# Optimization experiments

Measured on AMD Instinct MI355X. Metric: run time of the kernel, lower is better.

Reference implementation:

```python
import jax, jax.numpy as jnp
import numpy as np

DIM = 128
NUM_ROT = DIM * (DIM - 1) // 2  # 8128
# Strict upper-triangular pairs in row-major order: i outer, j from i+1 (matches the torch loop)
_PI, _PJ = np.triu_indices(DIM, k=1)


def setup_inputs() -> dict:
    key = jax.random.key(0)
    k1, k2 = jax.random.split(key)
    x = jax.random.normal(k1, (32, 4096, DIM), dtype=jnp.float32)
    angles = jax.random.normal(k2, (NUM_ROT,), dtype=jnp.float32) * 0.01
    bias = jnp.zeros((DIM,), dtype=jnp.float32)
    return {"x": x, "angles": angles, "bias": bias}


def reference(x, angles, bias):
    # Sequential Givens plane rotations applied in pair order (read-after-write chain),
    # expressed as a lax.scan carrying the full vector batch.
    cos_vals = jnp.cos(angles)
    sin_vals = jnp.sin(angles)
    ii = jnp.asarray(_PI, dtype=jnp.int32)
    jj = jnp.asarray(_PJ, dtype=jnp.int32)

    def step(out, cs):
        c, s, i, j = cs
        xi = out[..., i]  # [B, S]
        xj = out[..., j]
        out = out.at[..., i].set(c * xi - s * xj).at[..., j].set(s * xi + c * xj)
        return out, None

    out, _ = jax.lax.scan(step, x, (cos_vals, sin_vals, ii, jj))
    return out + bias
```

## Files before the change

kernel.cpp:

```cpp
#include <hip/hip_runtime.h>
#include <hip/hip_bf16.h>

#define DIM 128

typedef __attribute__((ext_vector_type(4))) float f32x4;
typedef __attribute__((ext_vector_type(8))) short bf16x8;

__device__ __forceinline__ unsigned short f2bf(float f) {
  union { float f; unsigned int u; } v; v.f = f;
  unsigned int u = v.u;
  return (unsigned short)((u + 0x7FFFu + ((u >> 16) & 1u)) >> 16);
}

template<int LO, int NF, int N, int RB, int RE>
__device__ void build_group(const float* __restrict__ angles, float* __restrict__ A,
                            float4* __restrict__ cs) {
  const int t = threadIdx.x;
  for (int r0 = RB + t; r0 < RE; r0 += 256) {
    int i = (int)floorf((255.0f - sqrtf(65025.0f - 8.0f * (float)r0)) * 0.5f);
    if (i < 0) i = 0; if (i > 126) i = 126;
    while (127 * (i + 1) - ((i + 1) * i) / 2 <= r0) ++i;
    while (127 * i - (i * (i - 1)) / 2 > r0) --i;
    const int Ti = 127 * i - (i * (i - 1)) / 2;
    const int j  = i + 1 + (r0 - Ti);
    const int fl = i - LO, p = fl >> 1, sec = fl & 1;
    const int f1 = 2 * p;
    const int off = p * (N - p) + ((j - LO) - f1 - 1);
    float s, c; __sincosf(angles[r0], &s, &c);
    float2 v; v.x = c; v.y = s;
    *((float2*)&cs[off] + sec) = v;
  }
  __syncthreads();
  if (t >= N) return;

  float col[N];
  #pragma unroll
  for (int r = 0; r < N; ++r) col[r] = (r == t) ? 1.0f : 0.0f;

  constexpr int P = (NF + 1) / 2;
  #pragma unroll
  for (int p = 0; p < P; ++p) {
    const int f1 = 2 * p;
    const float4 e0 = cs[p * (N - p)];
    float r1 = col[f1];
    const float rj = col[f1 + 1];
    float r2 = fmaf(e0.y, r1, e0.x * rj);
    r1 = fmaf(e0.x, r1, -(e0.y * rj));
    #pragma unroll
    for (int jl = f1 + 2; jl < N; ++jl) {
      const float4 e = cs[p * (N - p) + (jl - f1 - 1)];
      const float rv = col[jl];
      const float wv = fmaf(e.y, r1, e.x * rv);
      r1 = fmaf(e.x, r1, -(e.y * rv));
      col[jl] = fmaf(e.w, r2, e.z * wv);
      r2 = fmaf(e.z, r2, -(e.w * wv));
    }
    col[f1] = r1; col[f1 + 1] = r2;
  }
  #pragma unroll
  for (int r = 0; r < N; ++r) A[r * N + t] = col[r];
}

__global__ __launch_bounds__(256, 1) void k_build(const float* __restrict__ angles,
                                                  float* __restrict__ ws) {
  __shared__ float4 cs[1104];
  const int t = threadIdx.x;
  for (int k = t; k < 1104; k += 256) { float4 v; v.x = 1.f; v.y = 0.f; v.z = 1.f; v.w = 0.f; cs[k] = v; }
  __syncthreads();
  switch (blockIdx.x) {
    case 0: build_group<0, 17, 128,    0, 2023>(angles, ws,         cs); break;
    case 1: build_group<17, 21, 111, 2023, 4123>(angles, ws + 16384, cs); break;
    case 2: build_group<38, 26,  90, 4123, 6112>(angles, ws + 28705, cs); break;
    default: build_group<64, 63, 64, 6112, 8128>(angles, ws + 36805, cs); break;
  }
}

__global__ __launch_bounds__(128) void k_combine(const float* __restrict__ ws,
                                                 unsigned short* __restrict__ Mb) {
  __shared__ float x[DIM];
  const int c = blockIdx.x, r = threadIdx.x;
  x[r] = (r == c) ? 1.0f : 0.0f;
  __syncthreads();
  const int LOs[4]  = {0, 17, 38, 64};
  const int Ns[4]   = {128, 111, 90, 64};
  const int offs[4] = {0, 16384, 28705, 36805};
  #pragma unroll
  for (int g = 0; g < 4; ++g) {
    const int lo = LOs[g], n = Ns[g];
    float y;
    if (r >= lo) {
      const float* Ar = ws + offs[g] + (r - lo) * n;
      float acc = 0.0f;
      #pragma unroll 8
      for (int k = 0; k < n; ++k) acc = fmaf(Ar[k], x[lo + k], acc);
      y = acc;
    } else {
      y = x[r];
    }
    __syncthreads();
    x[r] = y;
    __syncthreads();
  }
  Mb[r * DIM + c] = f2bf(x[r]);
}

__global__ __launch_bounds__(256) void k_gemm(const float* __restrict__ X,
                                              const float* __restrict__ bias,
                                              const unsigned short* __restrict__ Mb,
                                              float* __restrict__ out) {
  const int lane = threadIdx.x & 63;
  const int wid  = threadIdx.x >> 6;
  const int l15  = lane & 15, lhi = lane >> 4;
  const int rowbase = blockIdx.x * 128 + wid * 32;

  f32x4 acc[2][8];
  #pragma unroll
  for (int m = 0; m < 2; ++m)
    #pragma unroll
    for (int n = 0; n < 8; ++n) acc[m][n] = (f32x4){0.f, 0.f, 0.f, 0.f};

  bf16x8 a[2][4];
  #pragma unroll
  for (int mt = 0; mt < 2; ++mt) {
    const float* xp = X + (rowbase + mt * 16 + l15) * DIM + lhi * 8;
    #pragma unroll
    for (int kt = 0; kt < 4; ++kt) {
      const f32x4 x0 = *(const f32x4*)(xp + kt * 32);
      const f32x4 x1 = *(const f32x4*)(xp + kt * 32 + 4);
      bf16x8 av;
      av[0] = (short)f2bf(x0[0]); av[1] = (short)f2bf(x0[1]);
      av[2] = (short)f2bf(x0[2]); av[3] = (short)f2bf(x0[3]);
      av[4] = (short)f2bf(x1[0]); av[5] = (short)f2bf(x1[1]);
      av[6] = (short)f2bf(x1[2]); av[7] = (short)f2bf(x1[3]);
      a[mt][kt] = av;
    }
  }

  #pragma unroll
  for (int kt = 0; kt < 4; ++kt) {
    #pragma unroll
    for (int n = 0; n < 8; ++n) {
      const bf16x8 b = *(const bf16x8*)(Mb + ((l15 + 16 * n) * DIM + kt * 32 + lhi * 8));
      acc[0][n] = __builtin_amdgcn_mfma_f32_16x16x32_bf16(a[0][kt], b, acc[0][n], 0, 0, 0);
      acc[1][n] = __builtin_amdgcn_mfma_f32_16x16x32_bf16(a[1][kt], b, acc[1][n], 0, 0, 0);
    }
  }

  #pragma unroll
  for (int n = 0; n < 8; ++n) {
    const float bs = bias[16 * n + l15];
    #pragma unroll
    for (int mt = 0; mt < 2; ++mt) {
      const int rb = rowbase + mt * 16 + lhi * 4;
      #pragma unroll
      for (int j = 0; j < 4; ++j)
        out[(rb + j) * DIM + 16 * n + l15] = acc[mt][n][j] + bs;
    }
  }
}

extern "C" void kernel_launch(void* const* d_in, const int* in_sizes, int n_in,
                              void* d_out, int out_size, void* d_ws, size_t ws_size,
                              hipStream_t stream) {
  const float* x      = (const float*)d_in[0];
  const float* angles = (const float*)d_in[1];
  const float* bias   = (const float*)d_in[2];
  float* out = (float*)d_out;
  float* ws  = (float*)d_ws;
  unsigned short* Mb = (unsigned short*)((char*)d_ws + 163616);

  k_build<<<4, 256, 0, stream>>>(angles, ws);
  k_combine<<<128, 128, 0, stream>>>(ws, Mb);
  k_gemm<<<1024, 256, 0, stream>>>(x, bias, Mb, out);
}
```

Baseline: 91.54 us.

## Stage X tile via LDS async loads and move build columns to shared memory

The GEMM kernel now copies each 128x128 fp32 X tile into LDS using global_load_lds with an XOR-swizzled layout, then reads the A fragments from LDS instead of making strided 16-byte global loads. The rotation-build kernel keeps each thread's column in shared memory instead of a fully unrolled register array, processing rotations in 16-wide chunks with a new padded coefficient layout. This aims to get coalesced global reads in the GEMM and to cut register pressure and code size in the build. The cost is 64KB of LDS per GEMM block, which limits occupancy, and an extra barrier before compute starts.

```diff
diff --git a/kernel.cpp b/kernel.cpp
--- a/kernel.cpp
+++ b/kernel.cpp
@@ -12,10 +12,24 @@
   return (unsigned short)((u + 0x7FFFu + ((u >> 16) & 1u)) >> 16);
 }
 
-template<int LO, int NF, int N, int RB, int RE>
+__device__ __forceinline__ void load_lds16(const float* src, float* dst) {
+  __builtin_amdgcn_global_load_lds((const __attribute__((address_space(1))) void*)src,
+                                   (__attribute__((address_space(3))) void*)dst, 16, 0, 0);
+}
+
+__device__ __forceinline__ int pair_start(int p) { return 2 * p + ((p & 1) << 1); }
+__device__ __forceinline__ int pair_Lp(int N, int p) {
+  const int fp = (p & 1) ? 0 : 2;
+  const int len = N - 2 * p - 2;
+  return (fp + len + 15) & ~15;
+}
+
+template<int LO, int N, int P, int RB, int RE>
 __device__ void build_group(const float* __restrict__ angles, float* __restrict__ A,
-                            float4* __restrict__ cs) {
+                            float* __restrict__ col, float4* __restrict__ cs) {
   const int t = threadIdx.x;
+  for (int k = t; k < 1248; k += 256) { float4 v; v.x = 1.f; v.y = 0.f; v.z = 1.f; v.w = 0.f; cs[k] = v; }
+  __syncthreads();
   for (int r0 = RB + t; r0 < RE; r0 += 256) {
     int i = (int)floorf((255.0f - sqrtf(65025.0f - 8.0f * (float)r0)) * 0.5f);
     if (i < 0) i = 0; if (i > 126) i = 126;
@@ -24,54 +38,68 @@
     const int Ti = 127 * i - (i * (i - 1)) / 2;
     const int j  = i + 1 + (r0 - Ti);
     const int fl = i - LO, p = fl >> 1, sec = fl & 1;
-    const int f1 = 2 * p;
-    const int off = p * (N - p) + ((j - LO) - f1 - 1);
+    int bp = 0;
+    for (int q = 0; q < p; ++q) bp += 1 + pair_Lp(N, q);
     float s, c; __sincosf(angles[r0], &s, &c);
-    float2 v; v.x = c; v.y = s;
-    *((float2*)&cs[off] + sec) = v;
+    const int jloc = j - LO;
+    if (sec == 0 && jloc == 2 * p + 1) {
+      *(float2*)&cs[bp] = (float2){c, s};
+    } else {
+      const int slot = bp + 1 + (jloc - pair_start(p));
+      *((float2*)&cs[slot] + sec) = (float2){c, s};
+    }
   }
   __syncthreads();
   if (t >= N) return;
 
-  float col[N];
-  #pragma unroll
-  for (int r = 0; r < N; ++r) col[r] = (r == t) ? 1.0f : 0.0f;
-
-  constexpr int P = (NF + 1) / 2;
-  #pragma unroll
+  float* myc = col + t * 148;
+  for (int r = 0; r < 148; ++r) myc[r] = (r == t) ? 1.0f : 0.0f;
+
+  int base = 0;
+  #pragma unroll 1
   for (int p = 0; p < P; ++p) {
     const int f1 = 2 * p;
-    const float4 e0 = cs[p * (N - p)];
-    float r1 = col[f1];
-    const float rj = col[f1 + 1];
+    const int st = pair_start(p);
+    const int Lp = pair_Lp(N, p);
+    const float4 e0 = cs[base];
+    float r1 = myc[f1];
+    const float rj = myc[f1 + 1];
     float r2 = fmaf(e0.y, r1, e0.x * rj);
     r1 = fmaf(e0.x, r1, -(e0.y * rj));
-    #pragma unroll
-    for (int jl = f1 + 2; jl < N; ++jl) {
-      const float4 e = cs[p * (N - p) + (jl - f1 - 1)];
-      const float rv = col[jl];
-      const float wv = fmaf(e.y, r1, e.x * rv);
-      r1 = fmaf(e.x, r1, -(e.y * rv));
-      col[jl] = fmaf(e.w, r2, e.z * wv);
-      r2 = fmaf(e.z, r2, -(e.w * wv));
-    }
-    col[f1] = r1; col[f1 + 1] = r2;
-  }
-  #pragma unroll
-  for (int r = 0; r < N; ++r) A[r * N + t] = col[r];
+    #pragma unroll 1
+    for (int jb = 0; jb < Lp; jb += 16) {
+      f32x4 v[4]; float4 e[16];
+      #pragma unroll
+      for (int q = 0; q < 4; ++q) v[q] = *(f32x4*)&myc[st + jb + 4 * q];
+      #pragma unroll
+      for (int q = 0; q < 16; ++q) e[q] = cs[base + 1 + jb + q];
+      #pragma unroll
+      for (int q = 0; q < 16; ++q) {
+        const float rv = v[q >> 2][q & 3];
+        const float wv = fmaf(e[q].y, r1, e[q].x * rv);
+        r1 = fmaf(e[q].x, r1, -(e[q].y * rv));
+        v[q >> 2][q & 3] = fmaf(e[q].w, r2, e[q].z * wv);
+        r2 = fmaf(e[q].z, r2, -(e[q].w * wv));
+      }
+      #pragma unroll
+      for (int q = 0; q < 4; ++q) *(f32x4*)&myc[st + jb + 4 * q] = v[q];
+    }
+    myc[f1] = r1;
+    myc[f1 + 1] = r2;
+    base += 1 + Lp;
+  }
+  for (int r = 0; r < N; ++r) A[r * N + t] = myc[r];
 }
 
 __global__ __launch_bounds__(256, 1) void k_build(const float* __restrict__ angles,
                                                   float* __restrict__ ws) {
-  __shared__ float4 cs[1104];
-  const int t = threadIdx.x;
-  for (int k = t; k < 1104; k += 256) { float4 v; v.x = 1.f; v.y = 0.f; v.z = 1.f; v.w = 0.f; cs[k] = v; }
-  __syncthreads();
+  __shared__ float  col[128 * 148];
+  __shared__ float4 cs[1248];
   switch (blockIdx.x) {
-    case 0: build_group<0, 17, 128,    0, 2023>(angles, ws,         cs); break;
-    case 1: build_group<17, 21, 111, 2023, 4123>(angles, ws + 16384, cs); break;
-    case 2: build_group<38, 26,  90, 4123, 6112>(angles, ws + 28705, cs); break;
-    default: build_group<64, 63, 64, 6112, 8128>(angles, ws + 36805, cs); break;
+    case 0: build_group< 0, 128,  9,    0, 2023>(angles, ws,         col, cs); break;
+    case 1: build_group<17, 111, 11, 2023, 4123>(angles, ws + 16384, col, cs); break;
+    case 2: build_group<38,  90, 13, 4123, 6112>(angles, ws + 28705, col, cs); break;
+    default: build_group<64, 64, 32, 6112, 8128>(angles, ws + 36805, col, cs); break;
   }
 }
 
@@ -108,10 +136,20 @@
                                               const float* __restrict__ bias,
                                               const unsigned short* __restrict__ Mb,
                                               float* __restrict__ out) {
-  const int lane = threadIdx.x & 63;
-  const int wid  = threadIdx.x >> 6;
-  const int l15  = lane & 15, lhi = lane >> 4;
-  const int rowbase = blockIdx.x * 128 + wid * 32;
+  __shared__ float Xs[128 * 128];
+  const int t = threadIdx.x;
+  const int lane = t & 63, wid = t >> 6;
+  const int l15 = lane & 15, lhi = lane >> 4;
+  const float* Xblk = X + (size_t)blockIdx.x * 16384;
+
+  #pragma unroll
+  for (int it = 0; it < 16; ++it) {
+    const int g = (it * 4 + wid) * 64 + lane;
+    const int r = g >> 5, kc = g & 31;
+    const int pu = (kc >> 1) ^ (r & 15), h = kc & 1;
+    load_lds16(Xblk + r * 128 + pu * 8 + h * 4, &Xs[(it * 4 + wid) * 256]);
+  }
+  __syncthreads();
 
   f32x4 acc[2][8];
   #pragma unroll
@@ -122,11 +160,13 @@
   bf16x8 a[2][4];
   #pragma unroll
   for (int mt = 0; mt < 2; ++mt) {
-    const float* xp = X + (rowbase + mt * 16 + l15) * DIM + lhi * 8;
+    const int r = wid * 32 + mt * 16 + l15;
     #pragma unroll
     for (int kt = 0; kt < 4; ++kt) {
-      const f32x4 x0 = *(const f32x4*)(xp + kt * 32);
-      const f32x4 x1 = *(const f32x4*)(xp + kt * 32 + 4);
+      const int pu = (kt * 4 + lhi) ^ (r & 15);
+      const float* p = &Xs[r * 128 + pu * 8];
+      const f32x4 x0 = *(const f32x4*)p;
+      const f32x4 x1 = *(const f32x4*)(p + 4);
       bf16x8 av;
       av[0] = (short)f2bf(x0[0]); av[1] = (short)f2bf(x0[1]);
       av[2] = (short)f2bf(x0[2]); av[3] = (short)f2bf(x0[3]);
@@ -146,6 +186,7 @@
     }
   }
 
+  const int rowbase = blockIdx.x * 128 + wid * 32;
   #pragma unroll
   for (int n = 0; n < 8; ++n) {
     const float bs = bias[16 * n + l15];
```

Result: slower. 108.7 us (+18.7%).

## Split rotation matrix build into 32 groups and shrink GEMM tiles

Applied to the files above, without the earlier changes.

The Givens rotation chain is now split into 32 groups built in parallel blocks, up from 4, with each block's partial rotation matrix accumulated in shared memory. The output buffer serves as scratch for these partial matrices. k_combine now multiplies through 32 padded partial matrices using vectorized loads. The GEMM uses one 16-row tile per wave with more blocks and a higher occupancy hint. The aim is to cut the serial latency of the small-grid build kernel, in exchange for more combine steps and shared-memory traffic.

```diff
diff --git a/kernel.cpp b/kernel.cpp
--- a/kernel.cpp
+++ b/kernel.cpp
@@ -2,9 +2,20 @@
 #include <hip/hip_bf16.h>
 
 #define DIM 128
+#define G 32
 
 typedef __attribute__((ext_vector_type(4))) float f32x4;
 typedef __attribute__((ext_vector_type(8))) short bf16x8;
+
+__device__ const int LOt[G + 1] = {
+  0,2,4,6,8,10,13,15,17,19,22,24,27,29,32,35,37,40,43,46,49,53,56,60,64,68,72,77,82,88,95,105,127};
+__device__ const int RBt[G + 1] = {
+  0,253,502,747,988,1225,1573,1800,2023,2242,2563,2772,3078,3277,3568,3850,4033,4300,4558,4807,
+  5047,5353,5572,5850,6112,6358,6588,6853,7093,7348,7600,7875,8128};
+__device__ const int AOFFt[G + 1] = {
+  0,16384,32512,47888,63016,77416,91576,104916,118024,130456,142664,154112,164928,175432,185332,
+  194548,203476,211848,219592,227072,233960,240280,245980,251164,255788,259884,263484,266620,
+  269272,271480,273080,274268,274820};
 
 __device__ __forceinline__ unsigned short f2bf(float f) {
   union { float f; unsigned int u; } v; v.f = f;
@@ -12,90 +23,100 @@
   return (unsigned short)((u + 0x7FFFu + ((u >> 16) & 1u)) >> 16);
 }
 
-template<int LO, int NF, int N, int RB, int RE>
-__device__ void build_group(const float* __restrict__ angles, float* __restrict__ A,
-                            float4* __restrict__ cs) {
+__global__ __launch_bounds__(256) void k_build(const float* __restrict__ angles,
+                                               float* __restrict__ Ascr) {
+  __shared__ float  L[DIM * DIM];
+  __shared__ float4 cs[256];
+  const int g  = blockIdx.x;
+  const int lo = LOt[g], n = DIM - lo;
+  const int nf = LOt[g + 1] - lo;
+  const int P  = (nf + 1) >> 1;
+  const int rb = RBt[g], re = RBt[g + 1];
+  float* A = Ascr + AOFFt[g];
   const int t = threadIdx.x;
-  for (int r0 = RB + t; r0 < RE; r0 += 256) {
+
+  cs[t] = (float4){1.f, 0.f, 1.f, 0.f};
+  __syncthreads();
+
+  for (int r0 = rb + t; r0 < re; r0 += 256) {
     int i = (int)floorf((255.0f - sqrtf(65025.0f - 8.0f * (float)r0)) * 0.5f);
     if (i < 0) i = 0; if (i > 126) i = 126;
     while (127 * (i + 1) - ((i + 1) * i) / 2 <= r0) ++i;
     while (127 * i - (i * (i - 1)) / 2 > r0) --i;
     const int Ti = 127 * i - (i * (i - 1)) / 2;
     const int j  = i + 1 + (r0 - Ti);
-    const int fl = i - LO, p = fl >> 1, sec = fl & 1;
-    const int f1 = 2 * p;
-    const int off = p * (N - p) + ((j - LO) - f1 - 1);
+    const int fl = i - lo, p = fl >> 1, sec = fl & 1;
+    const int f1 = 2 * p, jl = j - lo;
+    const int base = p * (n - p);
     float s, c; __sincosf(angles[r0], &s, &c);
-    float2 v; v.x = c; v.y = s;
-    *((float2*)&cs[off] + sec) = v;
+    int slot, half;
+    if (sec == 0 && jl == f1 + 1) { slot = base; half = 0; }
+    else { slot = base + (jl - f1 - 1); half = sec; }
+    *((float2*)&cs[slot] + half) = (float2){c, s};
   }
   __syncthreads();
-  if (t >= N) return;
 
-  float col[N];
-  #pragma unroll
-  for (int r = 0; r < N; ++r) col[r] = (r == t) ? 1.0f : 0.0f;
-
-  constexpr int P = (NF + 1) / 2;
-  #pragma unroll
-  for (int p = 0; p < P; ++p) {
-    const int f1 = 2 * p;
-    const float4 e0 = cs[p * (N - p)];
-    float r1 = col[f1];
-    const float rj = col[f1 + 1];
-    float r2 = fmaf(e0.y, r1, e0.x * rj);
-    r1 = fmaf(e0.x, r1, -(e0.y * rj));
-    #pragma unroll
-    for (int jl = f1 + 2; jl < N; ++jl) {
-      const float4 e = cs[p * (N - p) + (jl - f1 - 1)];
-      const float rv = col[jl];
-      const float wv = fmaf(e.y, r1, e.x * rv);
-      r1 = fmaf(e.x, r1, -(e.y * rv));
-      col[jl] = fmaf(e.w, r2, e.z * wv);
-      r2 = fmaf(e.z, r2, -(e.w * wv));
+  if (t < n) {
+    const int c = t;
+    for (int r = 0; r < n; ++r) L[r * n + c] = (r == c) ? 1.0f : 0.0f;
+    for (int p = 0; p < P; ++p) {
+      const int f1 = 2 * p;
+      const int base = p * (n - p);
+      const float4 e0 = cs[base];
+      float r1 = L[f1 * n + c];
+      const float rj = L[(f1 + 1) * n + c];
+      float r2 = fmaf(e0.y, r1, e0.x * rj);
+      r1 = fmaf(e0.x, r1, -(e0.y * rj));
+      #pragma unroll 8
+      for (int jl = f1 + 2; jl < n; ++jl) {
+        const float4 e = cs[base + (jl - f1 - 1)];
+        const float rv = L[jl * n + c];
+        const float wv = fmaf(e.y, r1, e.x * rv);
+        r1 = fmaf(e.x, r1, -(e.y * rv));
+        L[jl * n + c] = fmaf(e.w, r2, e.z * wv);
+        r2 = fmaf(e.z, r2, -(e.w * wv));
+      }
+      L[f1 * n + c] = r1;
+      L[(f1 + 1) * n + c] = r2;
     }
-    col[f1] = r1; col[f1 + 1] = r2;
   }
-  #pragma unroll
-  for (int r = 0; r < N; ++r) A[r * N + t] = col[r];
-}
-
-__global__ __launch_bounds__(256, 1) void k_build(const float* __restrict__ angles,
-                                                  float* __restrict__ ws) {
-  __shared__ float4 cs[1104];
-  const int t = threadIdx.x;
-  for (int k = t; k < 1104; k += 256) { float4 v; v.x = 1.f; v.y = 0.f; v.z = 1.f; v.w = 0.f; cs[k] = v; }
   __syncthreads();
-  switch (blockIdx.x) {
-    case 0: build_group<0, 17, 128,    0, 2023>(angles, ws,         cs); break;
-    case 1: build_group<17, 21, 111, 2023, 4123>(angles, ws + 16384, cs); break;
-    case 2: build_group<38, 26,  90, 4123, 6112>(angles, ws + 28705, cs); break;
-    default: build_group<64, 63, 64, 6112, 8128>(angles, ws + 36805, cs); break;
+  const int np = (n + 3) & ~3;
+  if (t < np) {
+    for (int r = 0; r < n; ++r)
+      A[r * np + t] = (t < n) ? L[r * n + t] : 0.0f;
   }
 }
 
-__global__ __launch_bounds__(128) void k_combine(const float* __restrict__ ws,
+__global__ __launch_bounds__(128) void k_combine(const float* __restrict__ Ascr,
                                                  unsigned short* __restrict__ Mb) {
-  __shared__ float x[DIM];
+  __shared__ float x[256];
   const int c = blockIdx.x, r = threadIdx.x;
   x[r] = (r == c) ? 1.0f : 0.0f;
+  x[r + 128] = 0.0f;
   __syncthreads();
-  const int LOs[4]  = {0, 17, 38, 64};
-  const int Ns[4]   = {128, 111, 90, 64};
-  const int offs[4] = {0, 16384, 28705, 36805};
-  #pragma unroll
-  for (int g = 0; g < 4; ++g) {
-    const int lo = LOs[g], n = Ns[g];
-    float y;
+  #pragma unroll 1
+  for (int g = 0; g < G; ++g) {
+    const int lo = LOt[g];
+    const int n  = DIM - lo;
+    const int np = (n + 3) & ~3;
+    const int nq = np >> 2;
+    float y = x[r];
     if (r >= lo) {
-      const float* Ar = ws + offs[g] + (r - lo) * n;
-      float acc = 0.0f;
-      #pragma unroll 8
-      for (int k = 0; k < n; ++k) acc = fmaf(Ar[k], x[lo + k], acc);
-      y = acc;
-    } else {
-      y = x[r];
+      const f32x4* Ar = (const f32x4*)(Ascr + AOFFt[g] + (r - lo) * np);
+      f32x4 buf[32];
+      #pragma unroll
+      for (int q = 0; q < 32; ++q)
+        buf[q] = (q < nq) ? Ar[q] : (f32x4){0.f, 0.f, 0.f, 0.f};
+      float a0 = 0.f, a1 = 0.f, a2 = 0.f, a3 = 0.f;
+      #pragma unroll
+      for (int q = 0; q < 32; ++q) {
+        a0 = fmaf(buf[q][0], x[lo + 4 * q],     a0);
+        a1 = fmaf(buf[q][1], x[lo + 4 * q + 1], a1);
+        a2 = fmaf(buf[q][2], x[lo + 4 * q + 2], a2);
+        a3 = fmaf(buf[q][3], x[lo + 4 * q + 3], a3);
+      }
+      y = (a0 + a1) + (a2 + a3);
     }
     __syncthreads();
     x[r] = y;
@@ -104,58 +125,42 @@
   Mb[r * DIM + c] = f2bf(x[r]);
 }
 
-__global__ __launch_bounds__(256) void k_gemm(const float* __restrict__ X,
-                                              const float* __restrict__ bias,
-                                              const unsigned short* __restrict__ Mb,
-                                              float* __restrict__ out) {
-  const int lane = threadIdx.x & 63;
-  const int wid  = threadIdx.x >> 6;
-  const int l15  = lane & 15, lhi = lane >> 4;
-  const int rowbase = blockIdx.x * 128 + wid * 32;
+__global__ __launch_bounds__(256, 8) void k_gemm(const float* __restrict__ X,
+                                                 const float* __restrict__ bias,
+                                                 const unsigned short* __restrict__ Mb,
+                                                 float* __restrict__ out) {
+  const int lane = threadIdx.x & 63, wid = threadIdx.x >> 6;
+  const int l15 = lane & 15, lhi = lane >> 4;
+  const int rowbase = blockIdx.x * 64 + wid * 16;
 
-  f32x4 acc[2][8];
+  f32x4 acc[8];
   #pragma unroll
-  for (int m = 0; m < 2; ++m)
-    #pragma unroll
-    for (int n = 0; n < 8; ++n) acc[m][n] = (f32x4){0.f, 0.f, 0.f, 0.f};
+  for (int n = 0; n < 8; ++n) acc[n] = (f32x4){0.f, 0.f, 0.f, 0.f};
 
-  bf16x8 a[2][4];
-  #pragma unroll
-  for (int mt = 0; mt < 2; ++mt) {
-    const float* xp = X + (rowbase + mt * 16 + l15) * DIM + lhi * 8;
-    #pragma unroll
-    for (int kt = 0; kt < 4; ++kt) {
-      const f32x4 x0 = *(const f32x4*)(xp + kt * 32);
-      const f32x4 x1 = *(const f32x4*)(xp + kt * 32 + 4);
-      bf16x8 av;
-      av[0] = (short)f2bf(x0[0]); av[1] = (short)f2bf(x0[1]);
-      av[2] = (short)f2bf(x0[2]); av[3] = (short)f2bf(x0[3]);
-      av[4] = (short)f2bf(x1[0]); av[5] = (short)f2bf(x1[1]);
-      av[6] = (short)f2bf(x1[2]); av[7] = (short)f2bf(x1[3]);
-      a[mt][kt] = av;
-    }
-  }
-
+  const float* xp = X + (size_t)(rowbase + l15) * DIM + lhi * 8;
   #pragma unroll
   for (int kt = 0; kt < 4; ++kt) {
+    const f32x4 x0 = *(const f32x4*)(xp + kt * 32);
+    const f32x4 x1 = *(const f32x4*)(xp + kt * 32 + 4);
+    bf16x8 av;
+    av[0] = (short)f2bf(x0[0]); av[1] = (short)f2bf(x0[1]);
+    av[2] = (short)f2bf(x0[2]); av[3] = (short)f2bf(x0[3]);
+    av[4] = (short)f2bf(x1[0]); av[5] = (short)f2bf(x1[1]);
+    av[6] = (short)f2bf(x1[2]); av[7] = (short)f2bf(x1[3]);
     #pragma unroll
     for (int n = 0; n < 8; ++n) {
       const bf16x8 b = *(const bf16x8*)(Mb + ((l15 + 16 * n) * DIM + kt * 32 + lhi * 8));
-      acc[0][n] = __builtin_amdgcn_mfma_f32_16x16x32_bf16(a[0][kt], b, acc[0][n], 0, 0, 0);
-      acc[1][n] = __builtin_amdgcn_mfma_f32_16x16x32_bf16(a[1][kt], b, acc[1][n], 0, 0, 0);
+      acc[n] = __builtin_amdgcn_mfma_f32_16x16x32_bf16(av, b, acc[n], 0, 0, 0);
     }
   }
 
   #pragma unroll
   for (int n = 0; n < 8; ++n) {
     const float bs = bias[16 * n + l15];
+    const int rb = rowbase + lhi * 4;
     #pragma unroll
-    for (int mt = 0; mt < 2; ++mt) {
-      const int rb = rowbase + mt * 16 + lhi * 4;
-      #pragma unroll
-      for (int j = 0; j < 4; ++j)
-        out[(rb + j) * DIM + 16 * n + l15] = acc[mt][n][j] + bs;
-    }
+    for (int j = 0; j < 4; ++j)
+      out[(size_t)(rb + j) * DIM + 16 * n + l15] = acc[n][j] + bs;
   }
 }
 
@@ -165,11 +170,11 @@
   const float* x      = (const float*)d_in[0];
   const float* angles = (const float*)d_in[1];
   const float* bias   = (const float*)d_in[2];
-  float* out = (float*)d_out;
-  float* ws  = (float*)d_ws;
-  unsigned short* Mb = (unsigned short*)((char*)d_ws + 163616);
+  float* out  = (float*)d_out;
+  float* Ascr = (float*)d_out;
+  unsigned short* Mb = (unsigned short*)d_ws;
 
-  k_build<<<4, 256, 0, stream>>>(angles, ws);
-  k_combine<<<128, 128, 0, stream>>>(ws, Mb);
-  k_gemm<<<1024, 256, 0, stream>>>(x, bias, Mb, out);
+  k_build<<<G, 256, 0, stream>>>(angles, Ascr);
+  k_combine<<<128, 128, 0, stream>>>(Ascr, Mb);
+  k_gemm<<<2048, 256, 0, stream>>>(x, bias, Mb, out);
 }
```

Measured after the change: 244.7 us. 167% more time.
